# Kernel optimization log

Hardware: AMD Instinct MI355X
Metric: run time of the kernel (lower is better)

Reference implementation:

```python
import jax, jax.numpy as jnp
import numpy as np

NUM_NODES = 50000
NUM_EDGES = 400000
NUM_GRAPHS = 16


def _glorot(key, shape):
    fan_in, fan_out = shape[0], shape[1]
    lim = jnp.sqrt(6.0 / (fan_in + fan_out))
    return jax.random.uniform(key, shape, jnp.float32, -lim, lim)


def setup_inputs() -> dict:
    key = jax.random.key(0)
    ks = jax.random.split(key, 12)
    x = jax.random.normal(ks[0], (NUM_NODES, 3), jnp.float32)
    edge_index = jax.random.randint(ks[1], (2, NUM_EDGES), 0, NUM_NODES, jnp.int64)
    batch = jax.random.randint(ks[2], (NUM_NODES,), 0, NUM_GRAPHS, jnp.int64)
    return {
        "x": x,
        "edge_index": edge_index,
        "batch": batch,
        "W1": _glorot(ks[3], (3, 512)),   "b1": jnp.zeros((512,), jnp.float32),
        "W2": _glorot(ks[4], (512, 1024)), "b2": jnp.zeros((1024,), jnp.float32),
        "W3": _glorot(ks[5], (1024, 512)), "b3": jnp.zeros((512,), jnp.float32),
        "fcw1": _glorot(ks[6], (512, 128)), "fcb1": jnp.zeros((128,), jnp.float32),
        "fcw2": _glorot(ks[7], (128, 1)),   "fcb2": jnp.zeros((1,), jnp.float32),
    }


def _gcn_conv(x, W, b, row, col, n):
    # PyG GCNConv: h = x W; out_i = sum_{j->i} d_j^{-1/2} d_i^{-1/2} h_j + b
    # (row, col) already include self-loops; edge weights are 1.
    h = x @ W  # [N, out]
    deg = jnp.zeros((n,), h.dtype).at[col].add(1.0)  # in-degree incl. self-loop
    dis = jax.lax.rsqrt(deg)  # deg >= 1 thanks to self-loops
    norm = dis[row] * dis[col]  # [E]
    msgs = h[row] * norm[:, None]  # [E, out] gather
    return jax.ops.segment_sum(msgs, col, num_segments=n) + b


def reference(x, edge_index, batch, W1, b1, W2, b2, W3, b3, fcw1, fcb1, fcw2, fcb2):
    n = x.shape[0]
    loop = jnp.arange(n, dtype=edge_index.dtype)
    row = jnp.concatenate([edge_index[0], loop])  # source
    col = jnp.concatenate([edge_index[1], loop])  # target

    h = jax.nn.relu(_gcn_conv(x, W1, b1, row, col, n))
    h = jax.nn.relu(_gcn_conv(h, W2, b2, row, col, n))
    h = jax.nn.relu(_gcn_conv(h, W3, b3, row, col, n))

    # global mean pool over graphs in the batch
    sums = jax.ops.segment_sum(h, batch, num_segments=NUM_GRAPHS)  # [G, 512]
    cnts = jax.ops.segment_sum(jnp.ones((n,), h.dtype), batch, num_segments=NUM_GRAPHS)
    pooled = sums / jnp.maximum(cnts, 1.0)[:, None]

    out = jax.nn.relu(pooled @ fcw1 + fcb1)
    out = out @ fcw2 + fcb2  # [G, 1]
    return out
```

## Files before the change

### kernel.cpp

```cpp
#include <hip/hip_runtime.h>
#include <hip/hip_bf16.h>

#define NNODES 50000
#define NEDGES 400000
#define NGRAPH 16

typedef __attribute__((ext_vector_type(4))) float floatx4;
typedef __attribute__((ext_vector_type(8))) short short8;

typedef __attribute__((address_space(3))) unsigned int lds_uint;
typedef __attribute__((address_space(1))) const unsigned int gbl_uint;

__device__ __forceinline__ void load16_to_lds(const void* g, void* l) {
    __builtin_amdgcn_global_load_lds((gbl_uint*)g, (lds_uint*)l, 16, 0, 0);
}

__global__ __launch_bounds__(64) void zero_out_k(float* out, int n) {
    int i = blockIdx.x * 64 + threadIdx.x;
    if (i < n) out[i] = 0.0f;
}

__global__ __launch_bounds__(256) void init_k(int* deg_cnt, int* cursor,
                                              float* gsum, int* gcnt,
                                              const float* __restrict__ x,
                                              float4* __restrict__ xp, int n) {
    int i = blockIdx.x * 256 + threadIdx.x;
    if (i < n) {
        deg_cnt[i] = 0; cursor[i] = 0;
        xp[i] = make_float4(x[i * 3 + 0], x[i * 3 + 1], x[i * 3 + 2], 0.0f);
    }
    if (i < NGRAPH * 512) gsum[i] = 0.0f;
    if (i < NGRAPH) gcnt[i] = 0;
}

__global__ __launch_bounds__(256) void deg_k(const int* __restrict__ col,
                                             int* __restrict__ deg_cnt, int e) {
    int i = blockIdx.x * 256 + threadIdx.x;
    if (i < e) atomicAdd(&deg_cnt[col[i]], 1);
}

__global__ __launch_bounds__(256) void segsum_k(const int* __restrict__ cnt,
                                                int* __restrict__ segsum, int n) {
    __shared__ int sb[256];
    int seg = blockIdx.x;
    int base = seg * 1024;
    int t = threadIdx.x;
    int s = 0;
#pragma unroll
    for (int j = 0; j < 4; ++j) {
        int idx = base + t + j * 256;
        if (idx < n) s += cnt[idx];
    }
    sb[t] = s;
    __syncthreads();
    for (int off = 128; off > 0; off >>= 1) {
        if (t < off) sb[t] += sb[t + off];
        __syncthreads();
    }
    if (t == 0) segsum[seg] = sb[0];
}

__global__ __launch_bounds__(64) void segscan_k(const int* __restrict__ segsum,
                                                int* __restrict__ segbase,
                                                int* __restrict__ offs,
                                                int nseg, int n) {
    if (threadIdx.x == 0) {
        int run = 0;
        for (int s = 0; s < nseg; ++s) { segbase[s] = run; run += segsum[s]; }
        offs[n] = run;
    }
}

__global__ __launch_bounds__(1024) void offs_k(const int* __restrict__ cnt,
                                               const int* __restrict__ segbase,
                                               int* __restrict__ offs,
                                               float* __restrict__ dis, int n) {
    __shared__ int sb[1024];
    int seg = blockIdx.x;
    int t = threadIdx.x;
    int i = seg * 1024 + t;
    int c = (i < n) ? cnt[i] : 0;
    sb[t] = c;
    __syncthreads();
    for (int off = 1; off < 1024; off <<= 1) {
        int v = (t >= off) ? sb[t - off] : 0;
        __syncthreads();
        sb[t] += v;
        __syncthreads();
    }
    if (i < n) {
        offs[i] = segbase[seg] + sb[t] - c;
        dis[i]  = rsqrtf((float)(c + 1));
    }
}

__global__ __launch_bounds__(256) void scatter_k(const int* __restrict__ row,
                                                 const int* __restrict__ col,
                                                 const int* __restrict__ offs,
                                                 int* __restrict__ cursor,
                                                 int* __restrict__ ssrc,
                                                 float* __restrict__ sw,
                                                 const float* __restrict__ dis, int e) {
    int i = blockIdx.x * 256 + threadIdx.x;
    if (i >= e) return;
    int d = col[i];
    int p = offs[d] + atomicAdd(&cursor[d], 1);
    int s = row[i];
    ssrc[p] = s;
    sw[p]   = dis[s];
}

__global__ __launch_bounds__(256) void agg3_k(const float4* __restrict__ xp,
                                              float* __restrict__ out,
                                              const int* __restrict__ offs,
                                              const int* __restrict__ ssrc,
                                              const float* __restrict__ sw,
                                              const float* __restrict__ dis, int n) {
    int d = blockIdx.x * 256 + threadIdx.x;
    if (d >= n) return;
    float dd = dis[d];
    float4 xd = xp[d];
    float a0 = dd * xd.x, a1 = dd * xd.y, a2 = dd * xd.z;
    int beg = offs[d], end = offs[d + 1];
    for (int e = beg; e < end; ++e) {
        int s = ssrc[e];
        float w = sw[e];
        float4 q = xp[s];
        a0 += w * q.x; a1 += w * q.y; a2 += w * q.z;
    }
    out[d * 3 + 0] = dd * a0;
    out[d * 3 + 1] = dd * a1;
    out[d * 3 + 2] = dd * a2;
}

__global__ __launch_bounds__(256) void gemm1_k(const float* __restrict__ aggx,
                                               const float* __restrict__ W1,
                                               const float* __restrict__ b1,
                                               __hip_bfloat16* __restrict__ h1, int n) {
    int wave = threadIdx.x >> 6;
    int lane = threadIdx.x & 63;
    int d = blockIdx.x * 4 + wave;
    if (d >= n) return;
    float a0 = aggx[d * 3 + 0], a1 = aggx[d * 3 + 1], a2 = aggx[d * 3 + 2];
    int f0 = lane * 8;
    short8 ov;
#pragma unroll
    for (int j = 0; j < 8; ++j) {
        int f = f0 + j;
        float v = b1[f] + a0 * W1[f] + a1 * W1[512 + f] + a2 * W1[1024 + f];
        __hip_bfloat16 h = __float2bfloat16(fmaxf(v, 0.0f));
        ov[j] = *(short*)&h;
    }
    *(short8*)&h1[(size_t)d * 512 + f0] = ov;
}

__device__ inline float bs2f(short v) {
    return __uint_as_float(((unsigned int)(unsigned short)v) << 16);
}

__global__ __launch_bounds__(256) void agg512w_k(const __hip_bfloat16* __restrict__ in,
                                                 __hip_bfloat16* __restrict__ out,
                                                 const int* __restrict__ offs,
                                                 const int* __restrict__ ssrc,
                                                 const float* __restrict__ sw,
                                                 const float* __restrict__ dis,
                                                 const float* __restrict__ bias,
                                                 int relu, int n) {
    int wave = threadIdx.x >> 6;
    int lane = threadIdx.x & 63;
    int d = blockIdx.x * 4 + wave;
    if (d >= n) return;
    float dd = dis[d];
    short8 p = *(const short8*)&in[(size_t)d * 512 + lane * 8];
    float acc[8];
#pragma unroll
    for (int j = 0; j < 8; ++j) acc[j] = dd * bs2f(p[j]);

    int beg = offs[d], end = offs[d + 1];
    int e = beg;
    for (; e + 3 < end; e += 4) {
        int s0 = ssrc[e],     s1 = ssrc[e + 1];
        int s2 = ssrc[e + 2], s3 = ssrc[e + 3];
        float w0 = sw[e],     w1 = sw[e + 1];
        float w2 = sw[e + 2], w3 = sw[e + 3];
        short8 q0 = *(const short8*)&in[(size_t)s0 * 512 + lane * 8];
        short8 q1 = *(const short8*)&in[(size_t)s1 * 512 + lane * 8];
        short8 q2 = *(const short8*)&in[(size_t)s2 * 512 + lane * 8];
        short8 q3 = *(const short8*)&in[(size_t)s3 * 512 + lane * 8];
#pragma unroll
        for (int j = 0; j < 8; ++j) acc[j] += w0 * bs2f(q0[j]);
#pragma unroll
        for (int j = 0; j < 8; ++j) acc[j] += w1 * bs2f(q1[j]);
#pragma unroll
        for (int j = 0; j < 8; ++j) acc[j] += w2 * bs2f(q2[j]);
#pragma unroll
        for (int j = 0; j < 8; ++j) acc[j] += w3 * bs2f(q3[j]);
    }
    for (; e < end; ++e) {
        int s0 = ssrc[e];
        float w0 = sw[e];
        short8 q0 = *(const short8*)&in[(size_t)s0 * 512 + lane * 8];
#pragma unroll
        for (int j = 0; j < 8; ++j) acc[j] += w0 * bs2f(q0[j]);
    }

    short8 ov;
#pragma unroll
    for (int j = 0; j < 8; ++j) {
        float v = acc[j] * dd;
        if (bias) v += bias[lane * 8 + j];
        if (relu) v = fmaxf(v, 0.0f);
        __hip_bfloat16 h = __float2bfloat16(v);
        ov[j] = *(short*)&h;
    }
    *(short8*)&out[(size_t)d * 512 + lane * 8] = ov;
}

__global__ __launch_bounds__(256) void tcvt_k(const float* __restrict__ W2,
                                              __hip_bfloat16* __restrict__ w2t,
                                              const float* __restrict__ W3,
                                              __hip_bfloat16* __restrict__ w3t) {
    __shared__ float tile[32][33];
    int t = threadIdx.x;
    const float* W; __hip_bfloat16* Wt;
    int K, N, idx;
    if (blockIdx.x < 512) { W = W2; Wt = w2t; K = 512;  N = 1024; idx = blockIdx.x; }
    else                  { W = W3; Wt = w3t; K = 1024; N = 512;  idx = blockIdx.x - 512; }
    int nbn = N / 32;
    int bn = (idx % nbn) * 32;
    int bk = (idx / nbn) * 32;
    int c = t & 31, r0 = t >> 5;
#pragma unroll
    for (int j = 0; j < 4; ++j) {
        int r = r0 + j * 8;
        tile[r][c] = W[(size_t)(bk + r) * N + bn + c];
    }
    __syncthreads();
#pragma unroll
    for (int j = 0; j < 4; ++j) {
        int r = r0 + j * 8;
        Wt[(size_t)(bn + r) * K + bk + c] = __float2bfloat16(tile[c][r]);
    }
}

__global__ __launch_bounds__(512, 4) void mfma_gemm256_k(
        const __hip_bfloat16* __restrict__ A,
        const __hip_bfloat16* __restrict__ Bt,
        const float* __restrict__ bias,
        __hip_bfloat16* __restrict__ C,
        int M, int N, int K, int relu, int lnt) {
    __shared__ short smem[24576];

    int tid  = threadIdx.x;
    int lane = tid & 63;
    int wave = tid >> 6;
    int wm = wave >> 1;
    int wn = wave & 1;
    int fr = lane & 15;
    int l4 = lane >> 4;

    int nwg = gridDim.x;
    int wg  = (blockIdx.x & 7) * (nwg >> 3) + (blockIdx.x >> 3);
    int mt  = wg >> lnt;
    int nt  = wg & ((1 << lnt) - 1);
    int bm  = mt << 8;
    int bn  = nt << 7;

    int r = lane & 15;
    int s = lane >> 4;
    const __hip_bfloat16* ga0 = A  + (size_t)(bm + (2 * wave + 0) * 16 + r) * K + s * 8;
    const __hip_bfloat16* ga1 = A  + (size_t)(bm + (2 * wave + 1) * 16 + r) * K + s * 8;
    const __hip_bfloat16* gb  = Bt + (size_t)(bn + wave * 16 + r) * K + s * 8;

    floatx4 acc[4][4] = {};

    auto stage = [&](int p) {
        short* sp = &smem[p * 12288];
        load16_to_lds(ga0, sp + (2 * wave + 0) * 512);
        load16_to_lds(ga1, sp + (2 * wave + 1) * 512);
        load16_to_lds(gb,  sp + 8192 + wave * 512);
        ga0 += 32; ga1 += 32; gb += 32;
    };

    auto compute = [&](int p) {
        const short* sm = &smem[p * 12288];
        short8 af[4], bf[4];
#pragma unroll
        for (int mi = 0; mi < 4; ++mi)
            af[mi] = *(const short8*)&sm[(wm * 4 + mi) * 512 + lane * 8];
#pragma unroll
        for (int ni = 0; ni < 4; ++ni)
            bf[ni] = *(const short8*)&sm[8192 + (wn * 4 + ni) * 512 + lane * 8];
        __builtin_amdgcn_s_setprio(1);
#pragma unroll
        for (int mi = 0; mi < 4; ++mi)
#pragma unroll
            for (int ni = 0; ni < 4; ++ni)
                acc[mi][ni] = __builtin_amdgcn_mfma_f32_16x16x32_bf16(
                    af[mi], bf[ni], acc[mi][ni], 0, 0, 0);
        __builtin_amdgcn_s_setprio(0);
    };

    int KT = K >> 5;
    stage(0);
    for (int t = 0; t < KT; ++t) {
        int p = t & 1;
        __builtin_amdgcn_s_barrier();
        if (t + 1 < KT) {
            stage(p ^ 1);
            asm volatile("s_waitcnt vmcnt(3)" ::: "memory");
        } else {
            asm volatile("s_waitcnt vmcnt(0)" ::: "memory");
        }
        __builtin_amdgcn_s_barrier();
        compute(p);
    }

    short* Cs = smem;
#pragma unroll
    for (int h = 0; h < 2; ++h) {
        __builtin_amdgcn_s_barrier();
        if ((wm >> 1) == h) {
#pragma unroll
            for (int mi = 0; mi < 4; ++mi) {
#pragma unroll
                for (int ni = 0; ni < 4; ++ni) {
                    int lr = (wm & 1) * 64 + mi * 16 + l4 * 4;
                    int cc = wn * 64 + ni * 16 + fr;
                    float bv = bias ? bias[bn + cc] : 0.0f;
#pragma unroll
                    for (int q = 0; q < 4; ++q) {
                        float v = acc[mi][ni][q] + bv;
                        if (relu) v = fmaxf(v, 0.0f);
                        __hip_bfloat16 hh = __float2bfloat16(v);
                        Cs[(lr + q) * 136 + cc] = *(short*)&hh;
                    }
                }
            }
        }
        __builtin_amdgcn_s_barrier();
#pragma unroll
        for (int i = 0; i < 4; ++i) {
            int idx = tid + 512 * i;
            int rr = idx >> 4, c8 = idx & 15;
            int grow = bm + h * 128 + rr;
            if (grow < M)
                *(short8*)&C[(size_t)grow * N + bn + c8 * 8] =
                    *(const short8*)&Cs[rr * 136 + c8 * 8];
        }
    }
}

__global__ __launch_bounds__(256) void pool_k(const __hip_bfloat16* __restrict__ h,
                                              const int* __restrict__ batch,
                                              float* __restrict__ gsum,
                                              int* __restrict__ gcnt, int n) {
    __shared__ float ls[NGRAPH * 512];
    __shared__ int lcnt[NGRAPH];
    int t = threadIdx.x;
    for (int i = t; i < NGRAPH * 512; i += 256) ls[i] = 0.0f;
    if (t < NGRAPH) lcnt[t] = 0;
    __syncthreads();
    for (int d = blockIdx.x; d < n; d += gridDim.x) {
        int g = batch[d];
        if (t == 0) atomicAdd(&lcnt[g], 1);
        unsigned int q = *(const unsigned int*)&h[(size_t)d * 512 + 2 * t];
        ls[g * 512 + 2 * t]     += __uint_as_float((q & 0xffffu) << 16);
        ls[g * 512 + 2 * t + 1] += __uint_as_float((q >> 16) << 16);
    }
    __syncthreads();
    for (int i = t; i < NGRAPH * 512; i += 256) atomicAdd(&gsum[i], ls[i]);
    if (t < NGRAPH) atomicAdd(&gcnt[t], lcnt[t]);
}

__global__ __launch_bounds__(128) void fc_k(const float* __restrict__ gsum,
                                            const int* __restrict__ gcnt,
                                            const float* __restrict__ fcw1,
                                            const float* __restrict__ fcb1,
                                            const float* __restrict__ fcw2,
                                            const float* __restrict__ fcb2,
                                            float* __restrict__ out) {
    int g = blockIdx.x;
    int t = threadIdx.x;
    __shared__ float pooled[512];
    __shared__ float red[128];
    float inv = 1.0f / fmaxf((float)gcnt[g], 1.0f);
    for (int i = t; i < 512; i += 128) pooled[i] = gsum[g * 512 + i] * inv;
    __syncthreads();
    float sacc = fcb1[t];
    for (int k = 0; k < 512; ++k) sacc += pooled[k] * fcw1[k * 128 + t];
    sacc = fmaxf(sacc, 0.0f);
    red[t] = sacc * fcw2[t];
    __syncthreads();
    for (int off = 64; off > 0; off >>= 1) {
        if (t < off) red[t] += red[t + off];
        __syncthreads();
    }
    if (t == 0) out[g] = red[0] + fcb2[0];
}

extern "C" void kernel_launch(void* const* d_in, const int* in_sizes, int n_in,
                              void* d_out, int out_size, void* d_ws, size_t ws_size,
                              hipStream_t stream) {
    const float* x    = (const float*)d_in[0];
    const int*   ei   = (const int*)d_in[1];
    const int*   batch= (const int*)d_in[2];
    const float* W1   = (const float*)d_in[3];
    const float* b1   = (const float*)d_in[4];
    const float* W2   = (const float*)d_in[5];
    const float* b2   = (const float*)d_in[6];
    const float* W3   = (const float*)d_in[7];
    const float* b3   = (const float*)d_in[8];
    const float* fcw1 = (const float*)d_in[9];
    const float* fcb1 = (const float*)d_in[10];
    const float* fcw2 = (const float*)d_in[11];
    const float* fcb2 = (const float*)d_in[12];
    float* out = (float*)d_out;

    const int N = in_sizes[0] / 3;
    const int E = in_sizes[1] / 2;
    const int Mpad = (N + 255) & ~255;
    const int nseg = (N + 1023) / 1024;
    const int* row = ei;
    const int* col = ei + E;

    size_t used = 0;
    auto need = [&](size_t bytes) {
        size_t off = used;
        used += (bytes + 255) & ~(size_t)255;
        return off;
    };
    size_t o_deg  = need((size_t)N * 4);
    size_t o_cur  = need((size_t)N * 4);
    size_t o_dis  = need((size_t)N * 4);
    size_t o_offs = need((size_t)(N + 1) * 4);
    size_t o_seg  = need((size_t)nseg * 4);
    size_t o_segb = need((size_t)nseg * 4);
    size_t o_ssrc = need((size_t)E * 4);
    size_t o_sw   = need((size_t)E * 4);
    size_t o_xp   = need((size_t)N * 16);
    size_t o_aggx = need((size_t)N * 3 * 4);
    size_t o_gsum = need((size_t)NGRAPH * 512 * 4);
    size_t o_gcnt = need((size_t)NGRAPH * 4);
    size_t o_w2t  = need((size_t)512 * 1024 * 2);
    size_t o_w3t  = need((size_t)1024 * 512 * 2);
    size_t o_bufX = need((size_t)Mpad * 512 * 2);
    size_t o_bufY = need((size_t)Mpad * 512 * 2);
    size_t o_bufZ = need((size_t)Mpad * 1024 * 2);

    if (used > ws_size) {
        hipLaunchKernelGGL(zero_out_k, dim3((out_size + 63) / 64), dim3(64), 0, stream,
                           out, out_size);
        return;
    }

    char* base = (char*)d_ws;
    int*    deg_cnt = (int*)   (base + o_deg);
    int*    cursor  = (int*)   (base + o_cur);
    float*  dis     = (float*) (base + o_dis);
    int*    offs    = (int*)   (base + o_offs);
    int*    segsum  = (int*)   (base + o_seg);
    int*    segbase = (int*)   (base + o_segb);
    int*    ssrc    = (int*)   (base + o_ssrc);
    float*  sw      = (float*) (base + o_sw);
    float4* xp      = (float4*)(base + o_xp);
    float*  aggx    = (float*) (base + o_aggx);
    float*  gsum    = (float*) (base + o_gsum);
    int*    gcnt    = (int*)   (base + o_gcnt);
    __hip_bfloat16* w2t  = (__hip_bfloat16*)(base + o_w2t);
    __hip_bfloat16* w3t  = (__hip_bfloat16*)(base + o_w3t);
    __hip_bfloat16* bufX = (__hip_bfloat16*)(base + o_bufX);
    __hip_bfloat16* bufY = (__hip_bfloat16*)(base + o_bufY);
    __hip_bfloat16* bufZ = (__hip_bfloat16*)(base + o_bufZ);
    (void)n_in;

    int gN = (N + 255) / 256;
    int gE = (E + 255) / 256;
    int gW = (N + 3) / 4;
    int nrt = Mpad / 256;

    hipLaunchKernelGGL(init_k, dim3(gN), dim3(256), 0, stream, deg_cnt, cursor, gsum, gcnt, x, xp, N);
    hipLaunchKernelGGL(deg_k, dim3(gE), dim3(256), 0, stream, col, deg_cnt, E);
    hipLaunchKernelGGL(segsum_k, dim3(nseg), dim3(256), 0, stream, deg_cnt, segsum, N);
    hipLaunchKernelGGL(segscan_k, dim3(1), dim3(64), 0, stream, segsum, segbase, offs, nseg, N);
    hipLaunchKernelGGL(offs_k, dim3(nseg), dim3(1024), 0, stream, deg_cnt, segbase, offs, dis, N);
    hipLaunchKernelGGL(scatter_k, dim3(gE), dim3(256), 0, stream, row, col, offs, cursor, ssrc, sw, dis, E);

    hipLaunchKernelGGL(tcvt_k, dim3(1024), dim3(256), 0, stream, W2, w2t, W3, w3t);

    hipLaunchKernelGGL(agg3_k, dim3(gN), dim3(256), 0, stream, xp, aggx, offs, ssrc, sw, dis, N);
    hipLaunchKernelGGL(gemm1_k, dim3(gW), dim3(256), 0, stream, aggx, W1, b1, bufX, N);

    hipLaunchKernelGGL(agg512w_k, dim3(gW), dim3(256), 0, stream, bufX, bufY, offs, ssrc, sw, dis,
                       (const float*)nullptr, 0, N);
    hipLaunchKernelGGL(mfma_gemm256_k, dim3(nrt * 8), dim3(512), 0, stream,
                       bufY, w2t, b2, bufZ, N, 1024, 512, 1, 3);

    hipLaunchKernelGGL(mfma_gemm256_k, dim3(nrt * 4), dim3(512), 0, stream,
                       bufZ, w3t, (const float*)nullptr, bufX, N, 512, 1024, 0, 2);
    hipLaunchKernelGGL(agg512w_k, dim3(gW), dim3(256), 0, stream, bufX, bufY, offs, ssrc, sw, dis,
                       b3, 1, N);

    hipLaunchKernelGGL(pool_k, dim3(256), dim3(256), 0, stream, bufY, batch, gsum, gcnt, N);
    hipLaunchKernelGGL(fc_k, dim3(NGRAPH), dim3(128), 0, stream, gsum, gcnt, fcw1, fcb1, fcw2, fcb2, out);
}
```

Before: 613.1 us.

## Switch GEMM to 128x256 tiles with B fragments loaded directly into registers

The MFMA GEMM tile goes from 256x128 to 128x256, with waves arranged 2x4. Only the A tile is now staged through LDS. Each wave loads its B fragments straight from global memory into double-buffered registers, which removes the LDS traffic for B and shrinks shared memory. The trade-offs are higher register pressure (launch bounds lowered to 3 blocks per CU), uncoalesced direct global loads for B, and an extra barrier per k-step. The loop is also unrolled by two so the register buffers stay statically indexed.

```diff
diff --git a/kernel.cpp b/kernel.cpp
--- a/kernel.cpp
+++ b/kernel.cpp
@@ -243,89 +243,88 @@
     }
 }
 
-__global__ __launch_bounds__(512, 4) void mfma_gemm256_k(
+__global__ __launch_bounds__(512, 3) void mfma_gemm256_k(
         const __hip_bfloat16* __restrict__ A,
         const __hip_bfloat16* __restrict__ Bt,
         const float* __restrict__ bias,
         __hip_bfloat16* __restrict__ C,
         int M, int N, int K, int relu, int lnt) {
-    __shared__ short smem[24576];
+    __shared__ short smem[17408];
 
     int tid  = threadIdx.x;
     int lane = tid & 63;
     int wave = tid >> 6;
-    int wm = wave >> 1;
-    int wn = wave & 1;
+    int wm = wave >> 2;
+    int wn = wave & 3;
     int fr = lane & 15;
+    int kg = lane >> 4;
     int l4 = lane >> 4;
 
     int nwg = gridDim.x;
     int wg  = (blockIdx.x & 7) * (nwg >> 3) + (blockIdx.x >> 3);
     int mt  = wg >> lnt;
     int nt  = wg & ((1 << lnt) - 1);
-    int bm  = mt << 8;
-    int bn  = nt << 7;
-
-    int r = lane & 15;
-    int s = lane >> 4;
-    const __hip_bfloat16* ga0 = A  + (size_t)(bm + (2 * wave + 0) * 16 + r) * K + s * 8;
-    const __hip_bfloat16* ga1 = A  + (size_t)(bm + (2 * wave + 1) * 16 + r) * K + s * 8;
-    const __hip_bfloat16* gb  = Bt + (size_t)(bn + wave * 16 + r) * K + s * 8;
+    int bm  = mt << 7;
+    int bn  = nt << 8;
+
+    const __hip_bfloat16* pa = A + (size_t)(bm + wave * 16 + fr) * K + kg * 8;
+    const __hip_bfloat16* pb = Bt + (size_t)(bn + wn * 64 + fr) * K + kg * 8;
+    size_t bstr = (size_t)16 * K;
 
     floatx4 acc[4][4] = {};
-
-    auto stage = [&](int p) {
-        short* sp = &smem[p * 12288];
-        load16_to_lds(ga0, sp + (2 * wave + 0) * 512);
-        load16_to_lds(ga1, sp + (2 * wave + 1) * 512);
-        load16_to_lds(gb,  sp + 8192 + wave * 512);
-        ga0 += 32; ga1 += 32; gb += 32;
-    };
-
-    auto compute = [&](int p) {
-        const short* sm = &smem[p * 12288];
-        short8 af[4], bf[4];
-#pragma unroll
-        for (int mi = 0; mi < 4; ++mi)
-            af[mi] = *(const short8*)&sm[(wm * 4 + mi) * 512 + lane * 8];
-#pragma unroll
-        for (int ni = 0; ni < 4; ++ni)
-            bf[ni] = *(const short8*)&sm[8192 + (wn * 4 + ni) * 512 + lane * 8];
-        __builtin_amdgcn_s_setprio(1);
-#pragma unroll
-        for (int mi = 0; mi < 4; ++mi)
+    short8 bfr[2][4];
+    short8 af[4];
+
+    int KT = K >> 5;
+
+    load16_to_lds(pa, &smem[wave * 512]);
+#pragma unroll
+    for (int ni = 0; ni < 4; ++ni)
+        bfr[0][ni] = *(const short8*)(pb + (size_t)ni * bstr);
+
+    auto step = [&](int p, int t) __attribute__((always_inline)) {
+        int more = (t + 1 < KT);
+        if (more) {
+            int k1 = (t + 1) << 5;
+            load16_to_lds(pa + k1, &smem[(p ^ 1) * 4096 + wave * 512]);
 #pragma unroll
             for (int ni = 0; ni < 4; ++ni)
-                acc[mi][ni] = __builtin_amdgcn_mfma_f32_16x16x32_bf16(
-                    af[mi], bf[ni], acc[mi][ni], 0, 0, 0);
-        __builtin_amdgcn_s_setprio(0);
-    };
-
-    int KT = K >> 5;
-    stage(0);
-    for (int t = 0; t < KT; ++t) {
-        int p = t & 1;
-        __builtin_amdgcn_s_barrier();
-        if (t + 1 < KT) {
-            stage(p ^ 1);
-            asm volatile("s_waitcnt vmcnt(3)" ::: "memory");
+                bfr[p ^ 1][ni] = *(const short8*)(pb + (size_t)ni * bstr + k1);
+            asm volatile("s_waitcnt vmcnt(5)" ::: "memory");
         } else {
             asm volatile("s_waitcnt vmcnt(0)" ::: "memory");
         }
         __builtin_amdgcn_s_barrier();
-        compute(p);
+        const short* sm = &smem[p * 4096];
+#pragma unroll
+        for (int mi = 0; mi < 4; ++mi)
+            af[mi] = *(const short8*)&sm[(wm * 4 + mi) * 512 + lane * 8];
+        __builtin_amdgcn_s_setprio(1);
+#pragma unroll
+        for (int mi = 0; mi < 4; ++mi)
+#pragma unroll
+            for (int ni = 0; ni < 4; ++ni)
+                acc[mi][ni] = __builtin_amdgcn_mfma_f32_16x16x32_bf16(
+                    af[mi], bfr[p][ni], acc[mi][ni], 0, 0, 0);
+        __builtin_amdgcn_s_setprio(0);
+        __builtin_amdgcn_s_barrier();
+    };
+
+    for (int t = 0; t < KT; t += 2) {
+        step(0, t);
+        step(1, t + 1);
     }
 
     short* Cs = smem;
 #pragma unroll
     for (int h = 0; h < 2; ++h) {
         __builtin_amdgcn_s_barrier();
-        if ((wm >> 1) == h) {
+        if (wm == h) {
 #pragma unroll
             for (int mi = 0; mi < 4; ++mi) {
 #pragma unroll
                 for (int ni = 0; ni < 4; ++ni) {
-                    int lr = (wm & 1) * 64 + mi * 16 + l4 * 4;
+                    int lr = mi * 16 + l4 * 4;
                     int cc = wn * 64 + ni * 16 + fr;
                     float bv = bias ? bias[bn + cc] : 0.0f;
 #pragma unroll
@@ -333,7 +332,7 @@
                         float v = acc[mi][ni][q] + bv;
                         if (relu) v = fmaxf(v, 0.0f);
                         __hip_bfloat16 hh = __float2bfloat16(v);
-                        Cs[(lr + q) * 136 + cc] = *(short*)&hh;
+                        Cs[(lr + q) * 264 + cc] = *(short*)&hh;
                     }
                 }
             }
@@ -342,11 +341,11 @@
 #pragma unroll
         for (int i = 0; i < 4; ++i) {
             int idx = tid + 512 * i;
-            int rr = idx >> 4, c8 = idx & 15;
-            int grow = bm + h * 128 + rr;
+            int rr = idx >> 5, c8 = idx & 31;
+            int grow = bm + h * 64 + rr;
             if (grow < M)
                 *(short8*)&C[(size_t)grow * N + bn + c8 * 8] =
-                    *(const short8*)&Cs[rr * 136 + c8 * 8];
+                    *(const short8*)&Cs[rr * 264 + c8 * 8];
         }
     }
 }
@@ -477,7 +476,7 @@
     int gN = (N + 255) / 256;
     int gE = (E + 255) / 256;
     int gW = (N + 3) / 4;
-    int nrt = Mpad / 256;
+    int nmt = Mpad / 128;
 
     hipLaunchKernelGGL(init_k, dim3(gN), dim3(256), 0, stream, deg_cnt, cursor, gsum, gcnt, x, xp, N);
     hipLaunchKernelGGL(deg_k, dim3(gE), dim3(256), 0, stream, col, deg_cnt, E);
@@ -493,11 +492,11 @@
 
     hipLaunchKernelGGL(agg512w_k, dim3(gW), dim3(256), 0, stream, bufX, bufY, offs, ssrc, sw, dis,
                        (const float*)nullptr, 0, N);
-    hipLaunchKernelGGL(mfma_gemm256_k, dim3(nrt * 8), dim3(512), 0, stream,
-                       bufY, w2t, b2, bufZ, N, 1024, 512, 1, 3);
-
-    hipLaunchKernelGGL(mfma_gemm256_k, dim3(nrt * 4), dim3(512), 0, stream,
-                       bufZ, w3t, (const float*)nullptr, bufX, N, 512, 1024, 0, 2);
+    hipLaunchKernelGGL(mfma_gemm256_k, dim3(nmt * 4), dim3(512), 0, stream,
+                       bufY, w2t, b2, bufZ, N, 1024, 512, 1, 2);
+
+    hipLaunchKernelGGL(mfma_gemm256_k, dim3(nmt * 2), dim3(512), 0, stream,
+                       bufZ, w3t, (const float*)nullptr, bufX, N, 512, 1024, 0, 1);
     hipLaunchKernelGGL(agg512w_k, dim3(gW), dim3(256), 0, stream, bufX, bufY, offs, ssrc, sw, dis,
                        b3, 1, N);
 
```

Result: slower. 789.9 us (+28.8%).
